# Kernel optimization log

Measured on AMD Instinct MI355X. Metric: run time of the kernel, lower is better.

## Reference

```python
import jax, jax.numpy as jnp
import numpy as np

B, SD, AD, H, QE, NQ = 16384, 512, 64, 1024, 64, 64


def setup_inputs() -> dict:
    key = jax.random.key(0)
    ks = jax.random.split(key, 12)
    s = 0.02
    p = lambda k, shape: (jax.random.normal(k, shape, jnp.float32) * s)
    return {
        "state": jax.random.normal(ks[0], (B, SD), jnp.float32),
        "action": jax.random.normal(ks[1], (B, AD), jnp.float32),
        # twin critics: leading axis 2 stacks q1 / q2 parameters
        "W_e1": p(ks[2], (2, QE, 1)),      "b_e1": p(ks[3], (2, QE)),
        "W_e2": p(ks[4], (2, QE, QE)),     "b_e2": p(ks[5], (2, QE)),
        "W_f1": p(ks[6], (2, H, SD + AD)), "b_f1": p(ks[7], (2, H)),
        "g1": jnp.ones((2, H), jnp.float32),  "beta1": jnp.zeros((2, H), jnp.float32),
        "W_f2": p(ks[8], (2, H, H)),       "b_f2": p(ks[9], (2, H)),
        "g2": jnp.ones((2, H), jnp.float32),  "beta2": jnp.zeros((2, H), jnp.float32),
        "W_h": p(ks[10], (2, 1, H + QE)),  "b_h": p(ks[11], (2, 1)),
    }


def _layernorm(x, g, b, eps=1e-5):
    mu = x.mean(-1, keepdims=True)
    var = ((x - mu) ** 2).mean(-1, keepdims=True)
    return (x - mu) * jax.lax.rsqrt(var + eps) * g + b


def _qnet(state, action, W_e1, b_e1, W_e2, b_e2, W_f1, b_f1, g1, beta1,
          W_f2, b_f2, g2, beta2, W_h, b_h):
    # feature_net (eval mode: dropout is identity)
    x = jnp.concatenate([state, action], axis=-1)            # [B, SD+AD]
    h = jax.nn.relu(_layernorm(x @ W_f1.T + b_f1, g1, beta1))
    feat = jax.nn.relu(_layernorm(h @ W_f2.T + b_f2, g2, beta2))  # [B, H]
    # tau embedding (batch-independent -> compute once per quantile, not per sample)
    tau = (jnp.linspace(0.0, 1.0, NQ + 1)[:-1] + 1.0 / (2 * NQ))[:, None]  # [NQ,1]
    te = jax.nn.relu(tau @ W_e1.T + b_e1) @ W_e2.T + b_e2    # [NQ, QE]
    # head on concat([feat, te]) == linear split (exact same math as the 64-iter loop)
    q_feat = feat @ W_h[0, :H]                               # [B]
    q_tau = te @ W_h[0, H:]                                  # [NQ]
    return q_feat[:, None] + q_tau[None, :] + b_h[0]         # [B, NQ]


def reference(state, action, W_e1, b_e1, W_e2, b_e2, W_f1, b_f1, g1, beta1,
              W_f2, b_f2, g2, beta2, W_h, b_h):
    qnet = lambda *ps: _qnet(state, action, *ps)
    q = jax.vmap(qnet)(W_e1, b_e1, W_e2, b_e2, W_f1, b_f1, g1, beta1,
                       W_f2, b_f2, g2, beta2, W_h, b_h)      # [2, B, NQ]
    return q[0], q[1]
```

## Files before the change

### kernel.cpp

```cpp
#include <hip/hip_runtime.h>
#include <stdint.h>

#define BATCH 16384
#define SDIM 512
#define ADIM 64
#define XDIM 576
#define HDIM 1024
#define NQD 64
#define QED 64

typedef __attribute__((ext_vector_type(8))) short short8;
typedef __attribute__((ext_vector_type(4))) float f32x4;

static __device__ inline unsigned short f2bf(float f) {
  unsigned int u = __float_as_uint(f);
  unsigned int r = (u + 0x7fffu + ((u >> 16) & 1u)) >> 16;
  return (unsigned short)r;
}
static __device__ inline float bf2f(unsigned short u) {
  return __uint_as_float(((unsigned int)u) << 16);
}

static __device__ inline void gload_lds16(const void* g, void* l) {
  __builtin_amdgcn_global_load_lds(
      (const __attribute__((address_space(1))) uint32_t*)g,
      (__attribute__((address_space(3))) uint32_t*)l, 16, 0, 0);
}


__global__ __launch_bounds__(256) void prep(const float* __restrict__ st,
                                            const float* __restrict__ ac,
                                            unsigned short* __restrict__ xb,
                                            const float* __restrict__ w1s,
                                            unsigned short* __restrict__ w1d,
                                            const float* __restrict__ w2s,
                                            unsigned short* __restrict__ w2d) {
  const int nx = BATCH * XDIM / 4;
  const int n1 = 2 * HDIM * XDIM / 4;
  const int n2 = 2 * HDIM * HDIM / 4;
  for (int i = blockIdx.x * blockDim.x + threadIdx.x; i < nx + n1 + n2;
       i += gridDim.x * blockDim.x) {
    float4 v;
    unsigned short* dst;
    int di;
    if (i < nx) {
      const int e = i * 4;
      const int b = e / XDIM;
      const int j = e - b * XDIM;
      if (j < SDIM) v = *(const float4*)(st + (size_t)b * SDIM + j);
      else          v = *(const float4*)(ac + (size_t)b * ADIM + (j - SDIM));
      dst = xb; di = i;
    } else if (i < nx + n1) {
      di = i - nx; v = ((const float4*)w1s)[di]; dst = w1d;
    } else {
      di = i - nx - n1; v = ((const float4*)w2s)[di]; dst = w2d;
    }
    ushort4 o;
    o.x = f2bf(v.x); o.y = f2bf(v.y); o.z = f2bf(v.z); o.w = f2bf(v.w);
    ((ushort4*)dst)[di] = o;
  }
}


__global__ void qtau_kernel(const float* __restrict__ We1, const float* __restrict__ be1,
                            const float* __restrict__ We2, const float* __restrict__ be2,
                            const float* __restrict__ Wh,  const float* __restrict__ bh,
                            float* __restrict__ qtau) {
  const int c = blockIdx.x >> 6;
  const int nq = blockIdx.x & 63;
  const int q = threadIdx.x;
  const float tau = (float)nq / 64.0f + 0.0078125f;
  float acc = be2[c * 64 + q];
  for (int e = 0; e < 64; ++e) {
    const float t1 = fmaxf(tau * We1[c * 64 + e] + be1[c * 64 + e], 0.0f);
    acc += t1 * We2[(c * 64 + q) * 64 + e];
  }
  float v = acc * Wh[c * (HDIM + QED) + HDIM + q];
  #pragma unroll
  for (int off = 32; off; off >>= 1) v += __shfl_xor(v, off);
  if (q == 0) qtau[c * 64 + nq] = v + bh[c];
}


template <int K>
__global__ __launch_bounds__(512, 4) void gemm_mn(const unsigned short* __restrict__ A,
                                                  const unsigned short* __restrict__ W,
                                                  const float* __restrict__ bias,
                                                  unsigned short* __restrict__ C) {
  constexpr int NT = K / 32;
  __shared__ unsigned short As[2][256][32];
  __shared__ unsigned short Bs[2][128][32];

  const int tid  = threadIdx.x;
  const int lane = tid & 63;
  const int wave = tid >> 6;
  const int wm = wave >> 1;
  const int wn = wave & 1;

  const int bid = (int)blockIdx.x;
  const int logical = (bid & 7) * 64 + (bid >> 3);
  const int mBase = (logical >> 3) * 256;
  const int nBase = (logical & 7) * 128;

  auto stage = [&](int buf, int kt) {
    #pragma unroll
    for (int i = 0; i < 2; ++i) {
      const int flat = i * 512 + tid;
      const int row  = flat >> 2;
      const int ls   = (flat & 3) ^ ((row >> 1) & 3);
      gload_lds16(A + (size_t)(mBase + row) * K + kt * 32 + ls * 8,
                  &As[buf][0][0] + (size_t)flat * 8);
    }
    {
      const int row = tid >> 2;
      const int ls  = (tid & 3) ^ ((row >> 1) & 3);
      gload_lds16(W + (size_t)(nBase + row) * K + kt * 32 + ls * 8,
                  &Bs[buf][0][0] + (size_t)tid * 8);
    }
  };

  f32x4 acc[4][4];
  #pragma unroll
  for (int fm = 0; fm < 4; ++fm)
    #pragma unroll
    for (int fn = 0; fn < 4; ++fn) {
      f32x4 z = {0.f, 0.f, 0.f, 0.f};
      acc[fm][fn] = z;
    }

  stage(0, 0);
  __syncthreads();

  for (int t = 0; t < NT; ++t) {
    const int buf = t & 1;
    if (t + 1 < NT) stage(buf ^ 1, t + 1);

    short8 af[4], bf[4];
    #pragma unroll
    for (int fm = 0; fm < 4; ++fm) {
      const int r  = wm * 64 + fm * 16 + (lane & 15);
      const int ps = (lane >> 4) ^ ((r >> 1) & 3);
      af[fm] = *(const short8*)&As[buf][r][ps * 8];
    }
    #pragma unroll
    for (int fn = 0; fn < 4; ++fn) {
      const int r  = wn * 64 + fn * 16 + (lane & 15);
      const int ps = (lane >> 4) ^ ((r >> 1) & 3);
      bf[fn] = *(const short8*)&Bs[buf][r][ps * 8];
    }

    __builtin_amdgcn_s_setprio(1);
    #pragma unroll
    for (int fm = 0; fm < 4; ++fm)
      #pragma unroll
      for (int fn = 0; fn < 4; ++fn)
        acc[fm][fn] = __builtin_amdgcn_mfma_f32_16x16x32_bf16(af[fm], bf[fn],
                                                              acc[fm][fn], 0, 0, 0);
    __builtin_amdgcn_s_setprio(0);
    __syncthreads();
  }

  #pragma unroll
  for (int fm = 0; fm < 4; ++fm) {
    const int r0 = mBase + wm * 64 + fm * 16 + (lane >> 4) * 4;
    #pragma unroll
    for (int fn = 0; fn < 4; ++fn) {
      const int col = nBase + wn * 64 + fn * 16 + (lane & 15);
      const float bv = bias[col];
      #pragma unroll
      for (int j = 0; j < 4; ++j)
        C[(size_t)(r0 + j) * HDIM + col] = f2bf(acc[fm][fn][j] + bv);
    }
  }
}


template <bool HEAD>
__global__ __launch_bounds__(256) void ln_head(const unsigned short* __restrict__ X,
                                               const float* __restrict__ g,
                                               const float* __restrict__ bta,
                                               unsigned short* __restrict__ Y,
                                               const float* __restrict__ Wh,
                                               const float* __restrict__ qt,
                                               float* __restrict__ out) {
  const int b = blockIdx.x;
  const int tid = threadIdx.x;
  const int lane = tid & 63;
  const int wave = tid >> 6;
  __shared__ float rs_[4], rq_[4], rp_[4];

  const ushort4 xv = ((const ushort4*)(X + (size_t)b * HDIM))[tid];
  const float x0 = bf2f(xv.x), x1 = bf2f(xv.y), x2 = bf2f(xv.z), x3 = bf2f(xv.w);
  float s = x0 + x1 + x2 + x3;
  float q = x0 * x0 + x1 * x1 + x2 * x2 + x3 * x3;
  #pragma unroll
  for (int off = 32; off; off >>= 1) {
    s += __shfl_xor(s, off);
    q += __shfl_xor(q, off);
  }
  if (lane == 0) { rs_[wave] = s; rq_[wave] = q; }
  __syncthreads();
  s = rs_[0] + rs_[1] + rs_[2] + rs_[3];
  q = rq_[0] + rq_[1] + rq_[2] + rq_[3];
  const float mu = s * (1.0f / 1024.0f);
  const float var = q * (1.0f / 1024.0f) - mu * mu;
  const float rsig = rsqrtf(var + 1e-5f);

  const float4 gv = ((const float4*)g)[tid];
  const float4 bv = ((const float4*)bta)[tid];
  const float y0 = fmaxf((x0 - mu) * rsig * gv.x + bv.x, 0.0f);
  const float y1 = fmaxf((x1 - mu) * rsig * gv.y + bv.y, 0.0f);
  const float y2 = fmaxf((x2 - mu) * rsig * gv.z + bv.z, 0.0f);
  const float y3 = fmaxf((x3 - mu) * rsig * gv.w + bv.w, 0.0f);

  if constexpr (!HEAD) {
    ushort4 o;
    o.x = f2bf(y0); o.y = f2bf(y1); o.z = f2bf(y2); o.w = f2bf(y3);
    ((ushort4*)(Y + (size_t)b * HDIM))[tid] = o;
  } else {
    const float4 wv = ((const float4*)Wh)[tid];
    float p = y0 * wv.x + y1 * wv.y + y2 * wv.z + y3 * wv.w;
    #pragma unroll
    for (int off = 32; off; off >>= 1) p += __shfl_xor(p, off);
    if (lane == 0) rp_[wave] = p;
    __syncthreads();
    if (tid < 64) {
      const float qf = rp_[0] + rp_[1] + rp_[2] + rp_[3];
      out[(size_t)b * NQD + tid] = qf + qt[tid];
    }
  }
}


extern "C" void kernel_launch(void* const* d_in, const int* in_sizes, int n_in,
                              void* d_out, int out_size, void* d_ws, size_t ws_size,
                              hipStream_t stream) {
  (void)in_sizes; (void)n_in; (void)out_size; (void)ws_size;
  const float* state  = (const float*)d_in[0];
  const float* action = (const float*)d_in[1];
  const float* We1 = (const float*)d_in[2];
  const float* be1 = (const float*)d_in[3];
  const float* We2 = (const float*)d_in[4];
  const float* be2 = (const float*)d_in[5];
  const float* Wf1 = (const float*)d_in[6];
  const float* bW1 = (const float*)d_in[7];
  const float* g1  = (const float*)d_in[8];
  const float* bt1 = (const float*)d_in[9];
  const float* Wf2 = (const float*)d_in[10];
  const float* bW2 = (const float*)d_in[11];
  const float* g2  = (const float*)d_in[12];
  const float* bt2 = (const float*)d_in[13];
  const float* Wh  = (const float*)d_in[14];
  const float* bh  = (const float*)d_in[15];
  float* out = (float*)d_out;

  char* ws = (char*)d_ws;
  unsigned short* xb   = (unsigned short*)(ws);
  unsigned short* w1b  = (unsigned short*)(ws + 18874368);
  unsigned short* w2b  = (unsigned short*)(ws + 21233664);
  float*          qtw  = (float*)(ws + 25427968);
  unsigned short* ha   = (unsigned short*)(ws + 25428480);
  unsigned short* hb   = (unsigned short*)(ws + 58982912);

  prep<<<2048, 256, 0, stream>>>(state, action, xb, Wf1, w1b, Wf2, w2b);
  qtau_kernel<<<128, 64, 0, stream>>>(We1, be1, We2, be2, Wh, bh, qtw);

  for (int c = 0; c < 2; ++c) {
    gemm_mn<XDIM><<<512, 512, 0, stream>>>(
        xb, w1b + (size_t)c * HDIM * XDIM, bW1 + c * HDIM, ha);
    ln_head<false><<<BATCH, 256, 0, stream>>>(
        ha, g1 + c * HDIM, bt1 + c * HDIM, hb, nullptr, nullptr, nullptr);
    gemm_mn<HDIM><<<512, 512, 0, stream>>>(
        hb, w2b + (size_t)c * HDIM * HDIM, bW2 + c * HDIM, ha);
    ln_head<true><<<BATCH, 256, 0, stream>>>(
        ha, g2 + c * HDIM, bt2 + c * HDIM, nullptr,
        Wh + (size_t)c * (HDIM + QED), qtw + c * 64, out + (size_t)c * BATCH * NQD);
  }
}
```

Baseline: 213.5 us.

## Batch both twin critics into single GEMM and LayerNorm launches

```diff
diff --git a/kernel.cpp b/kernel.cpp
--- a/kernel.cpp
+++ b/kernel.cpp
@@ -83,10 +83,11 @@
 
 
 template <int K>
-__global__ __launch_bounds__(512, 4) void gemm_mn(const unsigned short* __restrict__ A,
-                                                  const unsigned short* __restrict__ W,
-                                                  const float* __restrict__ bias,
-                                                  unsigned short* __restrict__ C) {
+__global__ __launch_bounds__(512, 4) void gemm_bc(const unsigned short* __restrict__ Abase,
+                                                  size_t aCritStride,
+                                                  const unsigned short* __restrict__ Wbase,
+                                                  const float* __restrict__ biasBase,
+                                                  unsigned short* __restrict__ Cbase) {
   constexpr int NT = K / 32;
   __shared__ unsigned short As[2][256][32];
   __shared__ unsigned short Bs[2][128][32];
@@ -98,9 +99,17 @@
   const int wn = wave & 1;
 
   const int bid = (int)blockIdx.x;
-  const int logical = (bid & 7) * 64 + (bid >> 3);
-  const int mBase = (logical >> 3) * 256;
-  const int nBase = (logical & 7) * 128;
+  const int L = (bid & 7) * 128 + (bid >> 3);
+  const int n = L & 7;
+  const int cidx = (L >> 3) & 1;
+  const int m = L >> 4;
+  const int mBase = m * 256;
+  const int nBase = n * 128;
+
+  const unsigned short* A = Abase + aCritStride * (size_t)cidx;
+  const unsigned short* W = Wbase + (size_t)cidx * HDIM * K;
+  const float* bias = biasBase + cidx * HDIM;
+  unsigned short* C = Cbase + (size_t)cidx * BATCH * HDIM;
 
   auto stage = [&](int buf, int kt) {
     #pragma unroll
@@ -176,20 +185,26 @@
 
 
 template <bool HEAD>
-__global__ __launch_bounds__(256) void ln_head(const unsigned short* __restrict__ X,
-                                               const float* __restrict__ g,
-                                               const float* __restrict__ bta,
-                                               unsigned short* __restrict__ Y,
-                                               const float* __restrict__ Wh,
-                                               const float* __restrict__ qt,
-                                               float* __restrict__ out) {
-  const int b = blockIdx.x;
+__global__ __launch_bounds__(256) void ln_bc(const unsigned short* __restrict__ Xb,
+                                             const float* __restrict__ gB,
+                                             const float* __restrict__ btB,
+                                             unsigned short* __restrict__ Yb,
+                                             const float* __restrict__ WhB,
+                                             const float* __restrict__ qtB,
+                                             float* __restrict__ outB) {
+  const int gb = blockIdx.x;
+  const int c = gb >> 14;
+  const int row = gb & (BATCH - 1);
+  const unsigned short* X = Xb + ((size_t)c * BATCH + row) * HDIM;
+  const float* g   = gB + c * HDIM;
+  const float* bta = btB + c * HDIM;
+
   const int tid = threadIdx.x;
   const int lane = tid & 63;
   const int wave = tid >> 6;
   __shared__ float rs_[4], rq_[4], rp_[4];
 
-  const ushort4 xv = ((const ushort4*)(X + (size_t)b * HDIM))[tid];
+  const ushort4 xv = ((const ushort4*)X)[tid];
   const float x0 = bf2f(xv.x), x1 = bf2f(xv.y), x2 = bf2f(xv.z), x3 = bf2f(xv.w);
   float s = x0 + x1 + x2 + x3;
   float q = x0 * x0 + x1 * x1 + x2 * x2 + x3 * x3;
@@ -216,8 +231,9 @@
   if constexpr (!HEAD) {
     ushort4 o;
     o.x = f2bf(y0); o.y = f2bf(y1); o.z = f2bf(y2); o.w = f2bf(y3);
-    ((ushort4*)(Y + (size_t)b * HDIM))[tid] = o;
+    ((ushort4*)(Yb + ((size_t)c * BATCH + row) * HDIM))[tid] = o;
   } else {
+    const float* Wh = WhB + c * (HDIM + QED);
     const float4 wv = ((const float4*)Wh)[tid];
     float p = y0 * wv.x + y1 * wv.y + y2 * wv.z + y3 * wv.w;
     #pragma unroll
@@ -226,7 +242,7 @@
     __syncthreads();
     if (tid < 64) {
       const float qf = rp_[0] + rp_[1] + rp_[2] + rp_[3];
-      out[(size_t)b * NQD + tid] = qf + qt[tid];
+      outB[((size_t)c * BATCH + row) * NQD + tid] = qf + qtB[c * 64 + tid];
     }
   }
 }
@@ -260,20 +276,13 @@
   unsigned short* w2b  = (unsigned short*)(ws + 21233664);
   float*          qtw  = (float*)(ws + 25427968);
   unsigned short* ha   = (unsigned short*)(ws + 25428480);
-  unsigned short* hb   = (unsigned short*)(ws + 58982912);
+  unsigned short* hb   = (unsigned short*)(ws + 92537344);
 
   prep<<<2048, 256, 0, stream>>>(state, action, xb, Wf1, w1b, Wf2, w2b);
   qtau_kernel<<<128, 64, 0, stream>>>(We1, be1, We2, be2, Wh, bh, qtw);
 
-  for (int c = 0; c < 2; ++c) {
-    gemm_mn<XDIM><<<512, 512, 0, stream>>>(
-        xb, w1b + (size_t)c * HDIM * XDIM, bW1 + c * HDIM, ha);
-    ln_head<false><<<BATCH, 256, 0, stream>>>(
-        ha, g1 + c * HDIM, bt1 + c * HDIM, hb, nullptr, nullptr, nullptr);
-    gemm_mn<HDIM><<<512, 512, 0, stream>>>(
-        hb, w2b + (size_t)c * HDIM * HDIM, bW2 + c * HDIM, ha);
-    ln_head<true><<<BATCH, 256, 0, stream>>>(
-        ha, g2 + c * HDIM, bt2 + c * HDIM, nullptr,
-        Wh + (size_t)c * (HDIM + QED), qtw + c * 64, out + (size_t)c * BATCH * NQD);
-  }
-}
+  gemm_bc<XDIM><<<1024, 512, 0, stream>>>(xb, 0, w1b, bW1, ha);
+  ln_bc<false><<<2 * BATCH, 256, 0, stream>>>(ha, g1, bt1, hb, nullptr, nullptr, nullptr);
+  gemm_bc<HDIM><<<1024, 512, 0, stream>>>(hb, (size_t)BATCH * HDIM, w2b, bW2, ha);
+  ln_bc<true><<<2 * BATCH, 256, 0, stream>>>(ha, g2, bt2, nullptr, Wh, qtw, out);
+}
```

New measurement: 202.2 us. 5.3% less time.
